# Performance work log

Hardware: AMD Instinct MI355X
Metric: run time of the kernel (lower is better)

The kernel has to match this reference:

```python
import jax, jax.numpy as jnp
import numpy as np

NH0 = 8          # per-head channels (min(max(512//64,2),8))
NHEADS = 4       # assumed einpool head count == number of equivariant eqs
NSTACKS = 4      # max(min(8//2,4),1)
MARGIN = 8.0
F = NH0 * NHEADS  # 32


def _mlp2(x, w1, b1, w2, b2):
    # 2-layer MLP: Linear -> ReLU -> Linear (matches MLP with nlayers=2)
    return jnp.maximum(x @ w1 + b1, 0.0) @ w2 + b2


def _mixed_pool(h, mask):
    # h: (B,C,A,W,F), mask: (B,C,A,W,1)
    B, C, A, W, Fc = h.shape
    # sin-transformed multi-head equivariant einsum pool over axes (a,b)
    y = jnp.sin(h).reshape(B, C, A, W, NH0, NHEADS) * mask[..., None]
    e0 = y[..., 0]                                                        # identity head
    e1 = jnp.broadcast_to(jnp.sum(y[..., 1], axis=3, keepdims=True), e0.shape)  # sum over b
    e2 = jnp.broadcast_to(jnp.sum(y[..., 2], axis=2, keepdims=True), e0.shape)  # sum over a
    e3 = jnp.broadcast_to(jnp.sum(y[..., 3], axis=(2, 3), keepdims=True), e0.shape)  # sum over a,b
    h0 = jnp.concatenate([e0, e1, e2, e3], axis=-1)                       # (B,C,A,W,NH0*4)
    # cascaded 4-way max pool over b, a, C (equivalent to joint max), broadcast back
    h1 = jnp.broadcast_to(jnp.max(h, axis=(1, 2, 3), keepdims=True), h.shape)
    return jnp.concatenate([h0, h1], axis=-1)                             # (B,C,A,W,2F)


def setup_inputs() -> dict:
    key = jax.random.key(0)
    ks = jax.random.split(key, 16)
    B, C, A, W = 8, 24, 96, 96
    nh = 128
    x = jax.random.normal(ks[0], (B, C, A, W), jnp.float32)
    rows_len = jax.random.randint(ks[1], (B, C), 48, A + 1, jnp.int32)
    cols_len = jax.random.randint(ks[2], (B, C), 48, W + 1, jnp.int32)

    def lin(k, fi, fo):
        return jax.random.normal(k, (fi, fo), jnp.float32) / np.float32(np.sqrt(fi))

    inp = {
        'x': x, 'rows_len': rows_len, 'cols_len': cols_len,
        't0_w1': lin(ks[3], 1, nh), 't0_b1': jnp.zeros((nh,), jnp.float32),
        't0_w2': lin(ks[4], nh, F), 't0_b2': jnp.zeros((F,), jnp.float32),
        't_w1': jax.random.normal(ks[5], (NSTACKS, 2 * F, nh), jnp.float32) / np.float32(np.sqrt(2 * F)),
        't_b1': jnp.zeros((NSTACKS, nh), jnp.float32),
        't_w2': jax.random.normal(ks[6], (NSTACKS, nh, F), jnp.float32) / np.float32(np.sqrt(nh)),
        't_b2': jnp.zeros((NSTACKS, F), jnp.float32),
        'tout_w1': lin(ks[7], F, nh), 'tout_b1': jnp.zeros((nh,), jnp.float32),
        'tout_w2': lin(ks[8], nh, 2), 'tout_b2': jnp.zeros((2,), jnp.float32),
    }
    return inp


def reference(x, rows_len, cols_len, t0_w1, t0_b1, t0_w2, t0_b2,
              t_w1, t_b1, t_w2, t_b2, tout_w1, tout_b1, tout_w2, tout_b2):
    B, C, A, W = x.shape
    # ragged validity mask from per-matrix (rows, cols) lengths (nested-tensor pad)
    ra = jnp.arange(A, dtype=jnp.int32)
    rb = jnp.arange(W, dtype=jnp.int32)
    m = ((ra[:, None] < rows_len[..., None, None]) &
         (rb[None, :] < cols_len[..., None, None])).astype(x.dtype)      # (B,C,A,W)
    # per-matrix normalization over valid region (torch .std is unbiased)
    n = jnp.sum(m, axis=(-1, -2), keepdims=True)
    mean = jnp.sum(x * m, axis=(-1, -2), keepdims=True) / jnp.maximum(n, 1.0)
    var = jnp.sum(((x - mean) ** 2) * m, axis=(-1, -2), keepdims=True) / jnp.maximum(n - 1.0, 1.0)
    std = jnp.maximum(jnp.sqrt(var), 1e-12)
    h = (((x - mean) / std) * m)[..., None]                               # (B,C,A,W,1)
    mask = m[..., None]                                                   # (B,C,A,W,1)

    h = _mlp2(h, t0_w1, t0_b1, t0_w2, t0_b2)                              # (B,C,A,W,F)
    for i in range(NSTACKS):
        h = h * mask
        skip = h
        hp = _mixed_pool(h, mask)
        h = skip + _mlp2(hp, t_w1[i], t_b1[i], t_w2[i], t_b2[i])
        h = h * mask

    num = jnp.clip(jnp.sum(h * h, axis=(2, 3)), 1e-20, None)              # (B,C,F)
    den = jnp.clip(jnp.sum(mask, axis=(2, 3)), 1e-12, None)               # (B,C,1)
    h = jnp.sqrt(num / den)
    h = jnp.mean(h, axis=1)                                               # (B,F)
    out = MARGIN * jnp.tanh(_mlp2(h, tout_w1, tout_b1, tout_w2, tout_b2))  # (B,2)
    return out
```

## Files before the change

kernel.cpp:

```cpp
#include <hip/hip_runtime.h>
#include <math.h>
#include <float.h>

#define NB 8
#define NC 24
#define NA 96
#define NW 96
#define NF 32
#define NHID 128
#define AW (NA*NW)
#define NBC (NB*NC)
#define NEL ((size_t)NBC*AW)
#define HSTR 17

typedef float v2f __attribute__((ext_vector_type(2)));
typedef float f32x4 __attribute__((ext_vector_type(4)));
typedef short short8_t __attribute__((ext_vector_type(8)));
#ifndef __has_builtin
#define __has_builtin(x) 0
#endif
#if __has_builtin(__builtin_elementwise_fma)
#define PKFMA(a,b,c) __builtin_elementwise_fma((a),(b),(c))
#else
#define PKFMA(a,b,c) ((a)*(b)+(c))
#endif

union frag_u { unsigned int u[4]; short8_t s; };

__device__ __forceinline__ unsigned short bf16rne(float x) {
    unsigned int u = __float_as_uint(x);
    unsigned int r = u + 0x7fffu + ((u >> 16) & 1u);
    return (unsigned short)(r >> 16);
}
__device__ __forceinline__ float bf2f(unsigned short v) {
    return __uint_as_float(((unsigned int)v) << 16);
}
__device__ __forceinline__ unsigned fkey(float x) {
    unsigned u = __float_as_uint(x);
    return (u >> 31) ? ~u : (u | 0x80000000u);
}
__device__ __forceinline__ float funkey(unsigned k) {
    return (k >> 31) ? __uint_as_float(k ^ 0x80000000u) : __uint_as_float(~k);
}
__device__ __forceinline__ float grp16_sum(float v) {
    v += __shfl_xor(v, 1, 64);
    v += __shfl_xor(v, 2, 64);
    v += __shfl_xor(v, 4, 64);
    v += __shfl_xor(v, 8, 64);
    return v;
}
__device__ __forceinline__ float grp16_max(float v) {
    v = fmaxf(v, __shfl_xor(v, 1, 64));
    v = fmaxf(v, __shfl_xor(v, 2, 64));
    v = fmaxf(v, __shfl_xor(v, 4, 64));
    v = fmaxf(v, __shfl_xor(v, 8, 64));
    return v;
}

__global__ __launch_bounds__(256) void stats_kernel(
    const float* __restrict__ x, const int* __restrict__ rows_len,
    const int* __restrict__ cols_len, float* __restrict__ stats)
{
    int bc = blockIdx.x;
    int R = rows_len[bc], L = cols_len[bc];
    const float* xp = x + (size_t)bc * AW;
    int n = R * L;
    float sx = 0.f, sxx = 0.f;
    for (int i = threadIdx.x; i < n; i += 256) {
        int a = i / L, w = i - a * L;
        float v = xp[a * NW + w];
        sx += v;
        sxx = fmaf(v, v, sxx);
    }
    __shared__ float r1[256], r2[256];
    r1[threadIdx.x] = sx; r2[threadIdx.x] = sxx;
    __syncthreads();
    for (int s = 128; s > 0; s >>= 1) {
        if (threadIdx.x < s) {
            r1[threadIdx.x] += r1[threadIdx.x + s];
            r2[threadIdx.x] += r2[threadIdx.x + s];
        }
        __syncthreads();
    }
    if (threadIdx.x == 0) {
        float fn = (float)n;
        float mean = r1[0] / fn;
        float var = fmaxf((r2[0] - r1[0] * r1[0] / fn) / (fn - 1.f), 0.f);
        float sd = fmaxf(sqrtf(var), 1e-12f);
        stats[2 * bc] = mean;
        stats[2 * bc + 1] = 1.f / sd;
    }
}

__global__ __launch_bounds__(256) void prep_kernel(
    const float* __restrict__ tw1, float* __restrict__ w1t)
{
    int i = blockIdx.x * 256 + threadIdx.x;
    if (i >= 4 * NHID * 24) return;
    int s = i / (NHID * 24), r = i % (NHID * 24);
    int j = r / 24, t = r % 24;
    w1t[i] = tw1[(size_t)s * 64 * NHID + t * NHID + j];
}

__global__ __launch_bounds__(256) void prep2_kernel(
    const float* __restrict__ tw2, unsigned short* __restrict__ w2bf)
{
    int i = blockIdx.x * 256 + threadIdx.x;
    if (i >= 4 * NF * NHID) return;
    int s = i / (NF * NHID), r = i % (NF * NHID);
    int f = r / NHID, j = r % NHID;
    float v = tw2[((size_t)s * NHID + j) * NF + f];
    unsigned short hi = bf16rne(v);
    float hf = bf2f(hi);
    unsigned short lo = bf16rne(v - hf);
    size_t base = (size_t)s * (2 * NF * NHID) + (size_t)f * NHID + j;
    w2bf[base] = hi;
    w2bf[base + NF * NHID] = lo;
}

__global__ __launch_bounds__(256, 4) void t0_kernel(
    const float* __restrict__ x, const int* __restrict__ rows_len,
    const int* __restrict__ cols_len, const float* __restrict__ stats,
    const float* __restrict__ w1, const float* __restrict__ b1,
    const float* __restrict__ w2, const float* __restrict__ b2,
    unsigned short* __restrict__ h, float* __restrict__ rowsum,
    float* __restrict__ colsum, float* __restrict__ matsum,
    unsigned* __restrict__ cmax_key)
{
    __shared__ float col_lds[96 * 9];
    __shared__ float row_lds[8 * 8];
    __shared__ float mat_lds[8];
    __shared__ unsigned max_lds[NF];

    int tid = threadIdx.x;
    int bc = blockIdx.x / 18;
    int base = (blockIdx.x % 18) * 512;
    int lane = tid & 63, wv = tid >> 6;
    int c16 = lane & 15;
    int R = rows_len[bc], L = cols_len[bc];
    float mean = stats[2 * bc], rstd = stats[2 * bc + 1];

    for (int i = tid; i < 96 * 9; i += 256) col_lds[i] = 0.f;
    if (tid < 64) row_lds[tid] = 0.f;
    if (tid < 8) mat_lds[tid] = 0.f;
    if (tid < NF) max_lds[tid] = 0u;

    int eA = base + wv * 128 + lane;
    int eB = eA + 64;
    int aA = eA / NW, wA = eA % NW;
    int aB = eB / NW, wB = eB % NW;
    bool vA = (aA < R) && (wA < L);
    bool vB = (aB < R) && (wB < L);
    size_t gA = (size_t)bc * AW + eA;
    float xA = vA ? (x[gA] - mean) * rstd : 0.f;
    float xB = vB ? (x[gA + 64] - mean) * rstd : 0.f;

    v2f oA[16], oB[16];
    const v2f* b22 = (const v2f*)b2;
    #pragma unroll
    for (int i = 0; i < 16; i++) { v2f bb = b22[i]; oA[i] = bb; oB[i] = bb; }
    for (int j = 0; j < NHID; j++) {
        float hA = fmaxf(fmaf(xA, w1[j], b1[j]), 0.f);
        float hB = fmaxf(fmaf(xB, w1[j], b1[j]), 0.f);
        const v2f* wr = (const v2f*)&w2[j * NF];
        v2f hA2 = {hA, hA}, hB2 = {hB, hB};
        #pragma unroll
        for (int i = 0; i < 16; i++) {
            v2f q = wr[i];
            oA[i] = PKFMA(hA2, q, oA[i]);
            oB[i] = PKFMA(hB2, q, oB[i]);
        }
    }
    float mA = vA ? 1.f : 0.f, mB = vB ? 1.f : 0.f;
    unsigned short* hp = h + (size_t)bc * NF * AW;
    #pragma unroll
    for (int f = 0; f < NF; f++) {
        hp[(size_t)f * AW + eA] = bf16rne(oA[f >> 1][f & 1] * mA);
        hp[(size_t)f * AW + eB] = bf16rne(oB[f >> 1][f & 1] * mB);
    }
    __syncthreads();

    int a0 = base / NW;
    int rowA = aA - a0, rowB = aB - a0;
    float matp[8];
    #pragma unroll
    for (int k = 0; k < 8; k++) matp[k] = 0.f;

    #pragma unroll
    for (int k = 0; k < 8; k++) {
        int fr = 4 * k + 1;
        float sA = grp16_sum(__sinf(oA[fr >> 1][fr & 1] * mA));
        float sB = grp16_sum(__sinf(oB[fr >> 1][fr & 1] * mB));
        if (c16 == 0) {
            atomicAdd(&row_lds[rowA * 8 + k], sA);
            atomicAdd(&row_lds[rowB * 8 + k], sB);
        }
        int fc = 4 * k + 2;
        atomicAdd(&col_lds[wA * 9 + k], __sinf(oA[fc >> 1][fc & 1] * mA));
        atomicAdd(&col_lds[wB * 9 + k], __sinf(oB[fc >> 1][fc & 1] * mB));
        int fm = 4 * k + 3;
        matp[k] = __sinf(oA[fm >> 1][fm & 1] * mA) + __sinf(oB[fm >> 1][fm & 1] * mB);
    }
    #pragma unroll
    for (int k = 0; k < 8; k++) {
        float v = grp16_sum(matp[k]);
        if (c16 == 0) atomicAdd(&mat_lds[k], v);
    }
    #pragma unroll
    for (int f = 0; f < NF; f++) {
        float v = grp16_max(fmaxf(oA[f >> 1][f & 1] * mA, oB[f >> 1][f & 1] * mB));
        if (c16 == 0) atomicMax(&max_lds[f], fkey(v));
    }
    __syncthreads();

    if (tid < 48) {
        int ar = a0 + (tid >> 3);
        if (ar < NA) atomicAdd(&rowsum[(bc * NA + ar) * 8 + (tid & 7)], row_lds[tid]);
    }
    if (tid < 8) atomicAdd(&matsum[bc * 8 + tid], mat_lds[tid]);
    if (tid >= 32 && tid < 64) atomicMax(&cmax_key[bc * NF + tid - 32], max_lds[tid - 32]);
    for (int i = tid; i < NW * 8; i += 256)
        atomicAdd(&colsum[bc * NW * 8 + i], col_lds[(i >> 3) * 9 + (i & 7)]);
}

__global__ __launch_bounds__(256) void precomp_kernel(
    const float* __restrict__ rowsum, const float* __restrict__ colsum,
    const float* __restrict__ matsum, const unsigned* __restrict__ cmax_key,
    const float* __restrict__ w1, const float* __restrict__ b1,
    float* __restrict__ rowc, float* __restrict__ colc)
{
    __shared__ float sbm[NF];
    __shared__ float sconst[NHID];
    __shared__ float scs[NW * 8];
    int tid = threadIdx.x;
    int bc = blockIdx.x, b = bc / NC;

    for (int i = tid; i < NW * 8; i += 256) scs[i] = colsum[bc * NW * 8 + i];
    if (tid < NF) {
        unsigned km = cmax_key[(b * NC) * NF + tid];
        for (int c = 1; c < NC; c++) {
            unsigned kc = cmax_key[(b * NC + c) * NF + tid];
            km = (kc > km) ? kc : km;
        }
        sbm[tid] = funkey(km);
    }
    __syncthreads();
    if (tid < NHID) {
        float v = b1[tid];
        const float* mp = matsum + bc * 8;
        #pragma unroll
        for (int k = 0; k < 8; k++) v = fmaf(mp[k], w1[(24 + k) * NHID + tid], v);
        #pragma unroll
        for (int f = 0; f < NF; f++) v = fmaf(sbm[f], w1[(32 + f) * NHID + tid], v);
        sconst[tid] = v;
    }
    __syncthreads();
    for (int i = tid; i < NHID * NA; i += 256) {
        int j = i / NA, aa = i - j * NA;
        const float* rp = rowsum + (bc * NA + aa) * 8;
        float v = sconst[j];
        #pragma unroll
        for (int k = 0; k < 8; k++) v = fmaf(rp[k], w1[(8 + k) * NHID + j], v);
        rowc[(size_t)bc * (NHID * NA) + i] = v;
    }
    for (int i = tid; i < NHID * NW; i += 256) {
        int j = i / NW, ww = i - j * NW;
        float v = 0.f;
        #pragma unroll
        for (int k = 0; k < 8; k++) v = fmaf(scs[ww * 8 + k], w1[(16 + k) * NHID + j], v);
        colc[(size_t)bc * (NHID * NW) + i] = v;
    }
}

__global__ __launch_bounds__(256, 4) void mlp_kernel(
    unsigned short* __restrict__ h, const float* __restrict__ rowc,
    const float* __restrict__ colc, const int* __restrict__ rows_len,
    const int* __restrict__ cols_len, const float* __restrict__ w1t,
    const unsigned short* __restrict__ w2bf, const float* __restrict__ b2,
    float* __restrict__ sqsum, float* __restrict__ rowsum,
    float* __restrict__ colsum, float* __restrict__ matsum,
    unsigned* __restrict__ cmax_key, int last, int do_pool)
{
    __shared__ unsigned int hid_hi[256 * HSTR];
    __shared__ unsigned int hid_lo[256 * HSTR];

    int tid = threadIdx.x;
    int bc = blockIdx.x / 36;
    int blk36 = blockIdx.x % 36;
    int base = blk36 * 256;
    int lane = tid & 63, wv = tid >> 6;
    int g = lane >> 4, c16 = lane & 15;

    int e = base + tid;
    int a = e / NW, wc = e - a * NW;
    unsigned short* hp = h + (size_t)bc * NF * AW;

    float p[8];
    #pragma unroll
    for (int k = 0; k < 8; k++) p[k] = __sinf(bf2f(hp[(size_t)(4 * k) * AW + e]));
    v2f p2[4];
    #pragma unroll
    for (int t = 0; t < 4; t++) p2[t] = (v2f){p[2 * t], p[2 * t + 1]};

    const unsigned short* w2hi = w2bf;
    const unsigned short* w2lo = w2bf + NF * NHID;

    f32x4 acc[4][2];
    #pragma unroll
    for (int t = 0; t < 2; t++) {
        f32x4 bb = *(const f32x4*)(b2 + 16 * t + 4 * g);
        #pragma unroll
        for (int ti = 0; ti < 4; ti++) acc[ti][t] = bb;
    }

    const float* rcr = rowc + (size_t)bc * (NHID * NA);
    const float* rcc = colc + (size_t)bc * (NHID * NW);

    for (int w = 0; w < 4; w++) {
        int jw = 32 * w;
        frag_u Ah[2], Al[2];
        #pragma unroll
        for (int t = 0; t < 2; t++) {
            size_t off = (size_t)(c16 + 16 * t) * NHID + jw + 8 * g;
            const unsigned int* ph = (const unsigned int*)(w2hi + off);
            const unsigned int* pl = (const unsigned int*)(w2lo + off);
            #pragma unroll
            for (int d = 0; d < 4; d++) { Ah[t].u[d] = ph[d]; Al[t].u[d] = pl[d]; }
        }

        #pragma unroll 4
        for (int jp = 0; jp < 16; jp++) {
            int jl = 2 * jp;
            const v2f* w1r0 = (const v2f*)(w1t + (size_t)(jw + jl) * 24);
            const v2f* w1r1 = w1r0 + 12;
            v2f u0 = {rcr[(size_t)(jw + jl) * NA + a], rcc[(size_t)(jw + jl) * NW + wc]};
            v2f u1 = {rcr[(size_t)(jw + jl + 1) * NA + a], rcc[(size_t)(jw + jl + 1) * NW + wc]};
            #pragma unroll
            for (int t = 0; t < 4; t++) {
                u0 = PKFMA(p2[t], w1r0[t], u0);
                u1 = PKFMA(p2[t], w1r1[t], u1);
            }
            float v0 = fmaxf(u0.x + u0.y, 0.f);
            float v1 = fmaxf(u1.x + u1.y, 0.f);
            unsigned int hi, lo;
            asm("v_cvt_pk_bf16_f32 %0, %1, %2" : "=v"(hi) : "v"(v0), "v"(v1));
            float h0 = __uint_as_float(hi << 16);
            float h1 = __uint_as_float(hi & 0xffff0000u);
            float l0 = v0 - h0, l1 = v1 - h1;
            asm("v_cvt_pk_bf16_f32 %0, %1, %2" : "=v"(lo) : "v"(l0), "v"(l1));
            hid_hi[tid * HSTR + jp] = hi;
            hid_lo[tid * HSTR + jp] = lo;
        }
        __syncthreads();

        #pragma unroll
        for (int ti = 0; ti < 4; ti++) {
            int el = (wv * 4 + ti) * 16 + c16;
            const unsigned int* bh = &hid_hi[el * HSTR + 4 * g];
            const unsigned int* bl = &hid_lo[el * HSTR + 4 * g];
            frag_u Bh, Bl;
            #pragma unroll
            for (int d = 0; d < 4; d++) { Bh.u[d] = bh[d]; Bl.u[d] = bl[d]; }
            #pragma unroll
            for (int t = 0; t < 2; t++) {
                acc[ti][t] = __builtin_amdgcn_mfma_f32_16x16x32_bf16(Ah[t].s, Bh.s, acc[ti][t], 0, 0, 0);
                acc[ti][t] = __builtin_amdgcn_mfma_f32_16x16x32_bf16(Al[t].s, Bh.s, acc[ti][t], 0, 0, 0);
                acc[ti][t] = __builtin_amdgcn_mfma_f32_16x16x32_bf16(Ah[t].s, Bl.s, acc[ti][t], 0, 0, 0);
            }
        }
        __syncthreads();
    }

    float* col_lds = (float*)hid_hi;
    float* row_lds = col_lds + 96 * 9;
    float* mat_lds = row_lds + 32;
    unsigned* max_lds = (unsigned*)(mat_lds + 8);
    if (do_pool) {
        for (int i = tid; i < 96 * 9 + 32 + 8 + 32; i += 256) col_lds[i] = 0.f;
        __syncthreads();
    }

    int R = rows_len[bc], L = cols_len[bc];
    int a0 = base / NW;
    float psum[2][4] = {{0.f, 0.f, 0.f, 0.f}, {0.f, 0.f, 0.f, 0.f}};
    float matp[2] = {0.f, 0.f};
    float mxp[2][4];
    #pragma unroll
    for (int t = 0; t < 2; t++)
        #pragma unroll
        for (int r = 0; r < 4; r++) mxp[t][r] = -FLT_MAX;

    #pragma unroll
    for (int ti = 0; ti < 4; ti++) {
        int el = (wv * 4 + ti) * 16 + c16;
        int ee = base + el;
        int aa = ee / NW, ww = ee - aa * NW;
        float mk = (aa < R && ww < L) ? 1.f : 0.f;
        float rowv[2];
        #pragma unroll
        for (int t = 0; t < 2; t++) {
            #pragma unroll
            for (int r = 0; r < 4; r++) {
                int f = 4 * g + r + 16 * t;
                unsigned short* ad = hp + (size_t)f * AW + ee;
                float hv = (bf2f(*ad) + acc[ti][t][r]) * mk;
                if (!last) *ad = bf16rne(hv);
                else       psum[t][r] = fmaf(hv, hv, psum[t][r]);
                if (do_pool) {
                    mxp[t][r] = fmaxf(mxp[t][r], hv);
                    if (r == 1)      rowv[t] = __sinf(hv);
                    else if (r == 2) atomicAdd(&col_lds[ww * 9 + g + 4 * t], __sinf(hv));
                    else if (r == 3) matp[t] += __sinf(hv);
                }
            }
        }
        if (do_pool) {
            #pragma unroll
            for (int t = 0; t < 2; t++) {
                float v = grp16_sum(rowv[t]);
                if (c16 == 0) atomicAdd(&row_lds[(aa - a0) * 8 + g + 4 * t], v);
            }
        }
    }

    if (do_pool) {
        #pragma unroll
        for (int t = 0; t < 2; t++) {
            float v = grp16_sum(matp[t]);
            if (c16 == 0) atomicAdd(&mat_lds[g + 4 * t], v);
            #pragma unroll
            for (int r = 0; r < 4; r++) {
                float m = grp16_max(mxp[t][r]);
                if (c16 == 0) atomicMax(&max_lds[4 * g + r + 16 * t], fkey(m));
            }
        }
        __syncthreads();
        if (tid < 32) {
            int ar = a0 + (tid >> 3);
            if (ar < NA) atomicAdd(&rowsum[(bc * NA + ar) * 8 + (tid & 7)], row_lds[tid]);
        }
        if (tid < 8) atomicAdd(&matsum[bc * 8 + tid], mat_lds[tid]);
        if (tid >= 32 && tid < 64) atomicMax(&cmax_key[bc * NF + tid - 32], max_lds[tid - 32]);
        for (int i = tid; i < NW * 8; i += 256)
            atomicAdd(&colsum[bc * NW * 8 + i], col_lds[(i >> 3) * 9 + (i & 7)]);
    }

    if (last) {
        float* sq_lds = (float*)hid_hi;
        if (tid < NF) sq_lds[tid] = 0.f;
        __syncthreads();
        #pragma unroll
        for (int t = 0; t < 2; t++) {
            #pragma unroll
            for (int r = 0; r < 4; r++) {
                float v = grp16_sum(psum[t][r]);
                if (c16 == 0) atomicAdd(&sq_lds[4 * g + r + 16 * t], v);
            }
        }
        __syncthreads();
        if (tid < NF) atomicAdd(&sqsum[bc * NF + tid], sq_lds[tid]);
    }
}

__global__ __launch_bounds__(64) void out_kernel(
    const float* __restrict__ sqsum, const int* __restrict__ rows_len,
    const int* __restrict__ cols_len, const float* __restrict__ w1,
    const float* __restrict__ b1, const float* __restrict__ w2,
    const float* __restrict__ b2, float* __restrict__ out)
{
    int b = threadIdx.x;
    if (b >= NB) return;
    float hm[NF];
    #pragma unroll
    for (int f = 0; f < NF; f++) hm[f] = 0.f;
    for (int c = 0; c < NC; c++) {
        int bc = b * NC + c;
        float n = (float)(rows_len[bc] * cols_len[bc]);
        float rdn = 1.f / fmaxf(n, 1e-12f);
        #pragma unroll
        for (int f = 0; f < NF; f++) {
            float q = fmaxf(sqsum[bc * NF + f], 1e-20f);
            hm[f] += sqrtf(q * rdn);
        }
    }
    #pragma unroll
    for (int f = 0; f < NF; f++) hm[f] *= (1.f / (float)NC);

    float o0 = b2[0], o1 = b2[1];
    for (int j = 0; j < NHID; j++) {
        float v = b1[j];
        #pragma unroll
        for (int f = 0; f < NF; f++) v = fmaf(hm[f], w1[f * NHID + j], v);
        v = fmaxf(v, 0.f);
        o0 = fmaf(v, w2[j * 2 + 0], o0);
        o1 = fmaf(v, w2[j * 2 + 1], o1);
    }
    out[b * 2 + 0] = 8.f * tanhf(o0);
    out[b * 2 + 1] = 8.f * tanhf(o1);
}

extern "C" void kernel_launch(void* const* d_in, const int* in_sizes, int n_in,
                              void* d_out, int out_size, void* d_ws, size_t ws_size,
                              hipStream_t stream)
{
    const float* x    = (const float*)d_in[0];
    const int* rl     = (const int*)d_in[1];
    const int* cl     = (const int*)d_in[2];
    const float* t0w1 = (const float*)d_in[3];
    const float* t0b1 = (const float*)d_in[4];
    const float* t0w2 = (const float*)d_in[5];
    const float* t0b2 = (const float*)d_in[6];
    const float* tw1  = (const float*)d_in[7];
    const float* tb1  = (const float*)d_in[8];
    const float* tw2  = (const float*)d_in[9];
    const float* tb2  = (const float*)d_in[10];
    const float* ow1  = (const float*)d_in[11];
    const float* ob1  = (const float*)d_in[12];
    const float* ow2  = (const float*)d_in[13];
    const float* ob2  = (const float*)d_in[14];
    float* out = (float*)d_out;

    float* ws    = (float*)d_ws;
    unsigned short* h = (unsigned short*)ws;
    float* stats = ws + NEL * NF;
    float*    rowb = stats + 2 * NBC;
    float*    matb = rowb + (size_t)NBC * NA * 8;
    unsigned* cmxb = (unsigned*)(matb + NBC * 8);
    float*    colb = (float*)(cmxb + NBC * NF);
    size_t    accum_floats = (size_t)NBC * NA * 8 + NBC * 8 + NBC * NF
                           + (size_t)NBC * NW * 8;
    float* sqb   = colb + (size_t)NBC * NW * 8;
    float* w1tb  = sqb + NBC * NF;
    float* rowcb = w1tb + 4 * NHID * 24;
    float* colcb = rowcb + (size_t)NBC * NHID * NA;
    unsigned short* w2bfb = (unsigned short*)(colcb + (size_t)NBC * NHID * NW);

    hipMemsetAsync(sqb, 0, NBC * NF * sizeof(float), stream);
    hipMemsetAsync(rowb, 0, accum_floats * sizeof(float), stream);
    stats_kernel<<<NBC, 256, 0, stream>>>(x, rl, cl, stats);
    prep_kernel<<<(4 * NHID * 24 + 255) / 256, 256, 0, stream>>>(tw1, w1tb);
    prep2_kernel<<<(4 * NF * NHID + 255) / 256, 256, 0, stream>>>(tw2, w2bfb);
    t0_kernel<<<(int)(NEL / 512), 256, 0, stream>>>(x, rl, cl, stats,
                                                    t0w1, t0b1, t0w2, t0b2, h,
                                                    rowb, colb, matb, cmxb);
    for (int s = 0; s < 4; s++) {
        precomp_kernel<<<NBC, 256, 0, stream>>>(rowb, colb, matb, cmxb,
            tw1 + (size_t)s * 64 * NHID, tb1 + s * NHID, rowcb, colcb);
        if (s < 3)
            hipMemsetAsync(rowb, 0, accum_floats * sizeof(float), stream);
        mlp_kernel<<<NBC * 36, 256, 0, stream>>>(h, rowcb, colcb, rl, cl,
            w1tb + (size_t)s * NHID * 24,
            w2bfb + (size_t)s * (2 * NF * NHID),
            tb2 + s * NF, sqb, rowb, colb, matb, cmxb,
            (s == 3) ? 1 : 0, (s < 3) ? 1 : 0);
    }
    out_kernel<<<1, 64, 0, stream>>>(sqb, rl, cl, ow1, ob1, ow2, ob2, out);
}
```

Baseline: 1.337 ms.

## Move t0 MLP second layer onto bf16 MFMA and specialize last stack kernel

The first-layer MLP kernel used to run its 128x32 second matmul as packed FP32 FMAs in registers, two elements per thread. It now stages the hidden activations in LDS as split hi/lo bf16 pairs and multiplies them with 3-term bf16 MFMA against pre-split t0_w2 weights, one element per thread with twice as many blocks. The stack MLP kernel is also split into separate mid and last variants, so the runtime do_pool and last branches go away and the last stack no longer writes h. The split-bf16 scheme keeps accuracy close to FP32, at the cost of extra LDS traffic and syncs in t0.

Result: faster. 1.201 ms, median of 2 (-10.2%).

```diff
diff --git a/kernel.cpp b/kernel.cpp
--- a/kernel.cpp
+++ b/kernel.cpp
@@ -56,6 +56,14 @@
     v = fmaxf(v, __shfl_xor(v, 8, 64));
     return v;
 }
+__device__ __forceinline__ void pack_hilo(float v0, float v1,
+                                          unsigned int& hi, unsigned int& lo) {
+    asm("v_cvt_pk_bf16_f32 %0, %1, %2" : "=v"(hi) : "v"(v0), "v"(v1));
+    float h0 = __uint_as_float(hi << 16);
+    float h1 = __uint_as_float(hi & 0xffff0000u);
+    float l0 = v0 - h0, l1 = v1 - h1;
+    asm("v_cvt_pk_bf16_f32 %0, %1, %2" : "=v"(lo) : "v"(l0), "v"(l1));
+}
 
 __global__ __launch_bounds__(256) void stats_kernel(
     const float* __restrict__ x, const int* __restrict__ rows_len,
@@ -111,109 +119,159 @@
     int f = r / NHID, j = r % NHID;
     float v = tw2[((size_t)s * NHID + j) * NF + f];
     unsigned short hi = bf16rne(v);
-    float hf = bf2f(hi);
-    unsigned short lo = bf16rne(v - hf);
+    unsigned short lo = bf16rne(v - bf2f(hi));
     size_t base = (size_t)s * (2 * NF * NHID) + (size_t)f * NHID + j;
     w2bf[base] = hi;
     w2bf[base + NF * NHID] = lo;
+}
+
+__global__ __launch_bounds__(256) void prep2t_kernel(
+    const float* __restrict__ t0w2, unsigned short* __restrict__ w2bf)
+{
+    int i = blockIdx.x * 256 + threadIdx.x;
+    if (i >= NF * NHID) return;
+    int f = i / NHID, j = i % NHID;
+    float v = t0w2[(size_t)j * NF + f];
+    unsigned short hi = bf16rne(v);
+    unsigned short lo = bf16rne(v - bf2f(hi));
+    w2bf[(size_t)f * NHID + j] = hi;
+    w2bf[(size_t)NF * NHID + f * NHID + j] = lo;
 }
 
 __global__ __launch_bounds__(256, 4) void t0_kernel(
     const float* __restrict__ x, const int* __restrict__ rows_len,
     const int* __restrict__ cols_len, const float* __restrict__ stats,
     const float* __restrict__ w1, const float* __restrict__ b1,
-    const float* __restrict__ w2, const float* __restrict__ b2,
+    const unsigned short* __restrict__ w2bf, const float* __restrict__ b2,
     unsigned short* __restrict__ h, float* __restrict__ rowsum,
     float* __restrict__ colsum, float* __restrict__ matsum,
     unsigned* __restrict__ cmax_key)
 {
-    __shared__ float col_lds[96 * 9];
-    __shared__ float row_lds[8 * 8];
-    __shared__ float mat_lds[8];
-    __shared__ unsigned max_lds[NF];
+    __shared__ unsigned int hid_hi[256 * HSTR];
+    __shared__ unsigned int hid_lo[256 * HSTR];
 
     int tid = threadIdx.x;
-    int bc = blockIdx.x / 18;
-    int base = (blockIdx.x % 18) * 512;
+    int bc = blockIdx.x / 36;
+    int blk36 = blockIdx.x % 36;
+    int base = blk36 * 256;
     int lane = tid & 63, wv = tid >> 6;
-    int c16 = lane & 15;
+    int g = lane >> 4, c16 = lane & 15;
+
+    int e = base + tid;
+    int a = e / NW, wc = e - a * NW;
     int R = rows_len[bc], L = cols_len[bc];
     float mean = stats[2 * bc], rstd = stats[2 * bc + 1];
-
-    for (int i = tid; i < 96 * 9; i += 256) col_lds[i] = 0.f;
-    if (tid < 64) row_lds[tid] = 0.f;
-    if (tid < 8) mat_lds[tid] = 0.f;
-    if (tid < NF) max_lds[tid] = 0u;
-
-    int eA = base + wv * 128 + lane;
-    int eB = eA + 64;
-    int aA = eA / NW, wA = eA % NW;
-    int aB = eB / NW, wB = eB % NW;
-    bool vA = (aA < R) && (wA < L);
-    bool vB = (aB < R) && (wB < L);
-    size_t gA = (size_t)bc * AW + eA;
-    float xA = vA ? (x[gA] - mean) * rstd : 0.f;
-    float xB = vB ? (x[gA + 64] - mean) * rstd : 0.f;
-
-    v2f oA[16], oB[16];
-    const v2f* b22 = (const v2f*)b2;
-    #pragma unroll
-    for (int i = 0; i < 16; i++) { v2f bb = b22[i]; oA[i] = bb; oB[i] = bb; }
-    for (int j = 0; j < NHID; j++) {
-        float hA = fmaxf(fmaf(xA, w1[j], b1[j]), 0.f);
-        float hB = fmaxf(fmaf(xB, w1[j], b1[j]), 0.f);
-        const v2f* wr = (const v2f*)&w2[j * NF];
-        v2f hA2 = {hA, hA}, hB2 = {hB, hB};
-        #pragma unroll
-        for (int i = 0; i < 16; i++) {
-            v2f q = wr[i];
-            oA[i] = PKFMA(hA2, q, oA[i]);
-            oB[i] = PKFMA(hB2, q, oB[i]);
-        }
-    }
-    float mA = vA ? 1.f : 0.f, mB = vB ? 1.f : 0.f;
+    bool valid = (a < R) && (wc < L);
+    float xn = valid ? (x[(size_t)bc * AW + e] - mean) * rstd : 0.f;
     unsigned short* hp = h + (size_t)bc * NF * AW;
-    #pragma unroll
-    for (int f = 0; f < NF; f++) {
-        hp[(size_t)f * AW + eA] = bf16rne(oA[f >> 1][f & 1] * mA);
-        hp[(size_t)f * AW + eB] = bf16rne(oB[f >> 1][f & 1] * mB);
-    }
+
+    const unsigned short* w2hi = w2bf;
+    const unsigned short* w2lo = w2bf + NF * NHID;
+
+    f32x4 acc[4][2];
+    #pragma unroll
+    for (int t = 0; t < 2; t++) {
+        f32x4 bb = *(const f32x4*)(b2 + 16 * t + 4 * g);
+        #pragma unroll
+        for (int ti = 0; ti < 4; ti++) acc[ti][t] = bb;
+    }
+
+    for (int w = 0; w < 4; w++) {
+        int jw = 32 * w;
+        frag_u Ah[2], Al[2];
+        #pragma unroll
+        for (int t = 0; t < 2; t++) {
+            size_t off = (size_t)(c16 + 16 * t) * NHID + jw + 8 * g;
+            const unsigned int* ph = (const unsigned int*)(w2hi + off);
+            const unsigned int* pl = (const unsigned int*)(w2lo + off);
+            #pragma unroll
+            for (int d = 0; d < 4; d++) { Ah[t].u[d] = ph[d]; Al[t].u[d] = pl[d]; }
+        }
+
+        #pragma unroll 4
+        for (int jp = 0; jp < 16; jp++) {
+            int j0 = jw + 2 * jp;
+            float v0 = fmaxf(fmaf(xn, w1[j0], b1[j0]), 0.f);
+            float v1 = fmaxf(fmaf(xn, w1[j0 + 1], b1[j0 + 1]), 0.f);
+            unsigned int hi, lo;
+            pack_hilo(v0, v1, hi, lo);
+            hid_hi[tid * HSTR + jp] = hi;
+            hid_lo[tid * HSTR + jp] = lo;
+        }
+        __syncthreads();
+
+        #pragma unroll
+        for (int ti = 0; ti < 4; ti++) {
+            int el = (wv * 4 + ti) * 16 + c16;
+            const unsigned int* bh = &hid_hi[el * HSTR + 4 * g];
+            const unsigned int* bl = &hid_lo[el * HSTR + 4 * g];
+            frag_u Bh, Bl;
+            #pragma unroll
+            for (int d = 0; d < 4; d++) { Bh.u[d] = bh[d]; Bl.u[d] = bl[d]; }
+            #pragma unroll
+            for (int t = 0; t < 2; t++) {
+                acc[ti][t] = __builtin_amdgcn_mfma_f32_16x16x32_bf16(Ah[t].s, Bh.s, acc[ti][t], 0, 0, 0);
+                acc[ti][t] = __builtin_amdgcn_mfma_f32_16x16x32_bf16(Al[t].s, Bh.s, acc[ti][t], 0, 0, 0);
+                acc[ti][t] = __builtin_amdgcn_mfma_f32_16x16x32_bf16(Ah[t].s, Bl.s, acc[ti][t], 0, 0, 0);
+            }
+        }
+        __syncthreads();
+    }
+
+    float* col_lds = (float*)hid_hi;
+    float* row_lds = col_lds + 96 * 9;
+    float* mat_lds = row_lds + 32;
+    unsigned* max_lds = (unsigned*)(mat_lds + 8);
+    for (int i = tid; i < 96 * 9 + 32 + 8 + 32; i += 256) col_lds[i] = 0.f;
     __syncthreads();
 
     int a0 = base / NW;
-    int rowA = aA - a0, rowB = aB - a0;
-    float matp[8];
-    #pragma unroll
-    for (int k = 0; k < 8; k++) matp[k] = 0.f;
-
-    #pragma unroll
-    for (int k = 0; k < 8; k++) {
-        int fr = 4 * k + 1;
-        float sA = grp16_sum(__sinf(oA[fr >> 1][fr & 1] * mA));
-        float sB = grp16_sum(__sinf(oB[fr >> 1][fr & 1] * mB));
-        if (c16 == 0) {
-            atomicAdd(&row_lds[rowA * 8 + k], sA);
-            atomicAdd(&row_lds[rowB * 8 + k], sB);
-        }
-        int fc = 4 * k + 2;
-        atomicAdd(&col_lds[wA * 9 + k], __sinf(oA[fc >> 1][fc & 1] * mA));
-        atomicAdd(&col_lds[wB * 9 + k], __sinf(oB[fc >> 1][fc & 1] * mB));
-        int fm = 4 * k + 3;
-        matp[k] = __sinf(oA[fm >> 1][fm & 1] * mA) + __sinf(oB[fm >> 1][fm & 1] * mB);
-    }
-    #pragma unroll
-    for (int k = 0; k < 8; k++) {
-        float v = grp16_sum(matp[k]);
-        if (c16 == 0) atomicAdd(&mat_lds[k], v);
-    }
-    #pragma unroll
-    for (int f = 0; f < NF; f++) {
-        float v = grp16_max(fmaxf(oA[f >> 1][f & 1] * mA, oB[f >> 1][f & 1] * mB));
-        if (c16 == 0) atomicMax(&max_lds[f], fkey(v));
-    }
-    __syncthreads();
-
-    if (tid < 48) {
+    float matp[2] = {0.f, 0.f};
+    float mxp[2][4];
+    #pragma unroll
+    for (int t = 0; t < 2; t++)
+        #pragma unroll
+        for (int r = 0; r < 4; r++) mxp[t][r] = -FLT_MAX;
+
+    #pragma unroll
+    for (int ti = 0; ti < 4; ti++) {
+        int el = (wv * 4 + ti) * 16 + c16;
+        int ee = base + el;
+        int aa = ee / NW, ww = ee - aa * NW;
+        float mk = (aa < R && ww < L) ? 1.f : 0.f;
+        float rowv[2];
+        #pragma unroll
+        for (int t = 0; t < 2; t++) {
+            #pragma unroll
+            for (int r = 0; r < 4; r++) {
+                int f = 4 * g + r + 16 * t;
+                float hv = acc[ti][t][r] * mk;
+                hp[(size_t)f * AW + ee] = bf16rne(hv);
+                mxp[t][r] = fmaxf(mxp[t][r], hv);
+                if (r == 1)      rowv[t] = __sinf(hv);
+                else if (r == 2) atomicAdd(&col_lds[ww * 9 + g + 4 * t], __sinf(hv));
+                else if (r == 3) matp[t] += __sinf(hv);
+            }
+        }
+        #pragma unroll
+        for (int t = 0; t < 2; t++) {
+            float v = grp16_sum(rowv[t]);
+            if (c16 == 0) atomicAdd(&row_lds[(aa - a0) * 8 + g + 4 * t], v);
+        }
+    }
+
+    #pragma unroll
+    for (int t = 0; t < 2; t++) {
+        float v = grp16_sum(matp[t]);
+        if (c16 == 0) atomicAdd(&mat_lds[g + 4 * t], v);
+        #pragma unroll
+        for (int r = 0; r < 4; r++) {
+            float m = grp16_max(mxp[t][r]);
+            if (c16 == 0) atomicMax(&max_lds[4 * g + r + 16 * t], fkey(m));
+        }
+    }
+    __syncthreads();
+    if (tid < 32) {
         int ar = a0 + (tid >> 3);
         if (ar < NA) atomicAdd(&rowsum[(bc * NA + ar) * 8 + (tid & 7)], row_lds[tid]);
     }
@@ -272,29 +330,14 @@
     }
 }
 
-__global__ __launch_bounds__(256, 4) void mlp_kernel(
-    unsigned short* __restrict__ h, const float* __restrict__ rowc,
-    const float* __restrict__ colc, const int* __restrict__ rows_len,
-    const int* __restrict__ cols_len, const float* __restrict__ w1t,
-    const unsigned short* __restrict__ w2bf, const float* __restrict__ b2,
-    float* __restrict__ sqsum, float* __restrict__ rowsum,
-    float* __restrict__ colsum, float* __restrict__ matsum,
-    unsigned* __restrict__ cmax_key, int last, int do_pool)
-{
-    __shared__ unsigned int hid_hi[256 * HSTR];
-    __shared__ unsigned int hid_lo[256 * HSTR];
-
-    int tid = threadIdx.x;
-    int bc = blockIdx.x / 36;
-    int blk36 = blockIdx.x % 36;
-    int base = blk36 * 256;
-    int lane = tid & 63, wv = tid >> 6;
-    int g = lane >> 4, c16 = lane & 15;
-
+__device__ __forceinline__ void mlp_core(
+    int tid, int bc, int base, int a, int wc, int g, int c16, int wv,
+    const unsigned short* hp, const float* rcr, const float* rcc,
+    const float* __restrict__ w1t, const unsigned short* __restrict__ w2bf,
+    const float* __restrict__ b2, unsigned int* hid_hi, unsigned int* hid_lo,
+    f32x4 (&acc)[4][2])
+{
     int e = base + tid;
-    int a = e / NW, wc = e - a * NW;
-    unsigned short* hp = h + (size_t)bc * NF * AW;
-
     float p[8];
     #pragma unroll
     for (int k = 0; k < 8; k++) p[k] = __sinf(bf2f(hp[(size_t)(4 * k) * AW + e]));
@@ -305,16 +348,12 @@
     const unsigned short* w2hi = w2bf;
     const unsigned short* w2lo = w2bf + NF * NHID;
 
-    f32x4 acc[4][2];
     #pragma unroll
     for (int t = 0; t < 2; t++) {
         f32x4 bb = *(const f32x4*)(b2 + 16 * t + 4 * g);
         #pragma unroll
         for (int ti = 0; ti < 4; ti++) acc[ti][t] = bb;
     }
-
-    const float* rcr = rowc + (size_t)bc * (NHID * NA);
-    const float* rcc = colc + (size_t)bc * (NHID * NW);
 
     for (int w = 0; w < 4; w++) {
         int jw = 32 * w;
@@ -343,11 +382,7 @@
             float v0 = fmaxf(u0.x + u0.y, 0.f);
             float v1 = fmaxf(u1.x + u1.y, 0.f);
             unsigned int hi, lo;
-            asm("v_cvt_pk_bf16_f32 %0, %1, %2" : "=v"(hi) : "v"(v0), "v"(v1));
-            float h0 = __uint_as_float(hi << 16);
-            float h1 = __uint_as_float(hi & 0xffff0000u);
-            float l0 = v0 - h0, l1 = v1 - h1;
-            asm("v_cvt_pk_bf16_f32 %0, %1, %2" : "=v"(lo) : "v"(l0), "v"(l1));
+            pack_hilo(v0, v1, hi, lo);
             hid_hi[tid * HSTR + jp] = hi;
             hid_lo[tid * HSTR + jp] = lo;
         }
@@ -370,19 +405,44 @@
         }
         __syncthreads();
     }
+}
+
+__global__ __launch_bounds__(256, 4) void mlp_mid_kernel(
+    unsigned short* __restrict__ h, const float* __restrict__ rowc,
+    const float* __restrict__ colc, const int* __restrict__ rows_len,
+    const int* __restrict__ cols_len, const float* __restrict__ w1t,
+    const unsigned short* __restrict__ w2bf, const float* __restrict__ b2,
+    float* __restrict__ rowsum, float* __restrict__ colsum,
+    float* __restrict__ matsum, unsigned* __restrict__ cmax_key)
+{
+    __shared__ unsigned int hid_hi[256 * HSTR];
+    __shared__ unsigned int hid_lo[256 * HSTR];
+
+    int tid = threadIdx.x;
+    int bc = blockIdx.x / 36;
+    int blk36 = blockIdx.x % 36;
+    int base = blk36 * 256;
+    int lane = tid & 63, wv = tid >> 6;
+    int g = lane >> 4, c16 = lane & 15;
+    int e = base + tid;
+    int a = e / NW, wc = e - a * NW;
+    unsigned short* hp = h + (size_t)bc * NF * AW;
+    const float* rcr = rowc + (size_t)bc * (NHID * NA);
+    const float* rcc = colc + (size_t)bc * (NHID * NW);
+
+    f32x4 acc[4][2];
+    mlp_core(tid, bc, base, a, wc, g, c16, wv, hp, rcr, rcc, w1t, w2bf, b2,
+             hid_hi, hid_lo, acc);
 
     float* col_lds = (float*)hid_hi;
     float* row_lds = col_lds + 96 * 9;
     float* mat_lds = row_lds + 32;
     unsigned* max_lds = (unsigned*)(mat_lds + 8);
-    if (do_pool) {
-        for (int i = tid; i < 96 * 9 + 32 + 8 + 32; i += 256) col_lds[i] = 0.f;
-        __syncthreads();
-    }
+    for (int i = tid; i < 96 * 9 + 32 + 8 + 32; i += 256) col_lds[i] = 0.f;
+    __syncthreads();
 
     int R = rows_len[bc], L = cols_len[bc];
     int a0 = base / NW;
-    float psum[2][4] = {{0.f, 0.f, 0.f, 0.f}, {0.f, 0.f, 0.f, 0.f}};
     float matp[2] = {0.f, 0.f};
     float mxp[2][4];
     #pragma unroll
@@ -404,62 +464,98 @@
                 int f = 4 * g + r + 16 * t;
                 unsigned short* ad = hp + (size_t)f * AW + ee;
                 float hv = (bf2f(*ad) + acc[ti][t][r]) * mk;
-                if (!last) *ad = bf16rne(hv);
-                else       psum[t][r] = fmaf(hv, hv, psum[t][r]);
-                if (do_pool) {
-                    mxp[t][r] = fmaxf(mxp[t][r], hv);
-                    if (r == 1)      rowv[t] = __sinf(hv);
-                    else if (r == 2) atomicAdd(&col_lds[ww * 9 + g + 4 * t], __sinf(hv));
-                    else if (r == 3) matp[t] += __sinf(hv);
-                }
+                *ad = bf16rne(hv);
+                mxp[t][r] = fmaxf(mxp[t][r], hv);
+                if (r == 1)      rowv[t] = __sinf(hv);
+                else if (r == 2) atomicAdd(&col_lds[ww * 9 + g + 4 * t], __sinf(hv));
+                else if (r == 3) matp[t] += __sinf(hv);
             }
         }
-        if (do_pool) {
-            #pragma unroll
-            for (int t = 0; t < 2; t++) {
-                float v = grp16_sum(rowv[t]);
-                if (c16 == 0) atomicAdd(&row_lds[(aa - a0) * 8 + g + 4 * t], v);
+        #pragma unroll
+        for (int t = 0; t < 2; t++) {
+            float v = grp16_sum(rowv[t]);
+            if (c16 == 0) atomicAdd(&row_lds[(aa - a0) * 8 + g + 4 * t], v);
+        }
+    }
+
+    #pragma unroll
+    for (int t = 0; t < 2; t++) {
+        float v = grp16_sum(matp[t]);
+        if (c16 == 0) atomicAdd(&mat_lds[g + 4 * t], v);
+        #pragma unroll
+        for (int r = 0; r < 4; r++) {
+            float m = grp16_max(mxp[t][r]);
+            if (c16 == 0) atomicMax(&max_lds[4 * g + r + 16 * t], fkey(m));
+        }
+    }
+    __syncthreads();
+    if (tid < 32) {
+        int ar = a0 + (tid >> 3);
+        if (ar < NA) atomicAdd(&rowsum[(bc * NA + ar) * 8 + (tid & 7)], row_lds[tid]);
+    }
+    if (tid < 8) atomicAdd(&matsum[bc * 8 + tid], mat_lds[tid]);
+    if (tid >= 32 && tid < 64) atomicMax(&cmax_key[bc * NF + tid - 32], max_lds[tid - 32]);
+    for (int i = tid; i < NW * 8; i += 256)
+        atomicAdd(&colsum[bc * NW * 8 + i], col_lds[(i >> 3) * 9 + (i & 7)]);
+}
+
+__global__ __launch_bounds__(256, 4) void mlp_last_kernel(
+    unsigned short* __restrict__ h, const float* __restrict__ rowc,
+    const float* __restrict__ colc, const int* __restrict__ rows_len,
+    const int* __restrict__ cols_len, const float* __restrict__ w1t,
+    const unsigned short* __restrict__ w2bf, const float* __restrict__ b2,
+    float* __restrict__ sqsum)
+{
+    __shared__ unsigned int hid_hi[256 * HSTR];
+    __shared__ unsigned int hid_lo[256 * HSTR];
+
+    int tid = threadIdx.x;
+    int bc = blockIdx.x / 36;
+    int blk36 = blockIdx.x % 36;
+    int base = blk36 * 256;
+    int lane = tid & 63, wv = tid >> 6;
+    int g = lane >> 4, c16 = lane & 15;
+    int e = base + tid;
+    int a = e / NW, wc = e - a * NW;
+    unsigned short* hp = h + (size_t)bc * NF * AW;
+    const float* rcr = rowc + (size_t)bc * (NHID * NA);
+    const float* rcc = colc + (size_t)bc * (NHID * NW);
+
+    f32x4 acc[4][2];
+    mlp_core(tid, bc, base, a, wc, g, c16, wv, hp, rcr, rcc, w1t, w2bf, b2,
+             hid_hi, hid_lo, acc);
+
+    int R = rows_len[bc], L = cols_len[bc];
+    float psum[2][4] = {{0.f, 0.f, 0.f, 0.f}, {0.f, 0.f, 0.f, 0.f}};
+    #pragma unroll
+    for (int ti = 0; ti < 4; ti++) {
+        int el = (wv * 4 + ti) * 16 + c16;
+        int ee = base + el;
+        int aa = ee / NW, ww = ee - aa * NW;
+        float mk = (aa < R && ww < L) ? 1.f : 0.f;
+        #pragma unroll
+        for (int t = 0; t < 2; t++) {
+            #pragma unroll
+            for (int r = 0; r < 4; r++) {
+                int f = 4 * g + r + 16 * t;
+                float hv = (bf2f(hp[(size_t)f * AW + ee]) + acc[ti][t][r]) * mk;
+                psum[t][r] = fmaf(hv, hv, psum[t][r]);
             }
         }
     }
-
-    if (do_pool) {
-        #pragma unroll
-        for (int t = 0; t < 2; t++) {
-            float v = grp16_sum(matp[t]);
-            if (c16 == 0) atomicAdd(&mat_lds[g + 4 * t], v);
-            #pragma unroll
-            for (int r = 0; r < 4; r++) {
-                float m = grp16_max(mxp[t][r]);
-                if (c16 == 0) atomicMax(&max_lds[4 * g + r + 16 * t], fkey(m));
-            }
-        }
-        __syncthreads();
-        if (tid < 32) {
-            int ar = a0 + (tid >> 3);
-            if (ar < NA) atomicAdd(&rowsum[(bc * NA + ar) * 8 + (tid & 7)], row_lds[tid]);
-        }
-        if (tid < 8) atomicAdd(&matsum[bc * 8 + tid], mat_lds[tid]);
-        if (tid >= 32 && tid < 64) atomicMax(&cmax_key[bc * NF + tid - 32], max_lds[tid - 32]);
-        for (int i = tid; i < NW * 8; i += 256)
-            atomicAdd(&colsum[bc * NW * 8 + i], col_lds[(i >> 3) * 9 + (i & 7)]);
-    }
-
-    if (last) {
-        float* sq_lds = (float*)hid_hi;
-        if (tid < NF) sq_lds[tid] = 0.f;
-        __syncthreads();
-        #pragma unroll
-        for (int t = 0; t < 2; t++) {
-            #pragma unroll
-            for (int r = 0; r < 4; r++) {
-                float v = grp16_sum(psum[t][r]);
-                if (c16 == 0) atomicAdd(&sq_lds[4 * g + r + 16 * t], v);
-            }
-        }
-        __syncthreads();
-        if (tid < NF) atomicAdd(&sqsum[bc * NF + tid], sq_lds[tid]);
-    }
+    float* sq_lds = (float*)hid_hi;
+    if (tid < NF) sq_lds[tid] = 0.f;
+    __syncthreads();
+    #pragma unroll
+    for (int t = 0; t < 2; t++) {
+        #pragma unroll
+        for (int r = 0; r < 4; r++) {
+            float v = grp16_sum(psum[t][r]);
+            if (c16 == 0) atomicAdd(&sq_lds[4 * g + r + 16 * t], v);
+        }
+    }
+    __syncthreads();
+    if (tid < NF) atomicAdd(&sqsum[bc * NF + tid], sq_lds[tid]);
 }
 
 __global__ __launch_bounds__(64) void out_kernel(
@@ -534,25 +630,32 @@
     float* rowcb = w1tb + 4 * NHID * 24;
     float* colcb = rowcb + (size_t)NBC * NHID * NA;
     unsigned short* w2bfb = (unsigned short*)(colcb + (size_t)NBC * NHID * NW);
+    unsigned short* w2t0b = w2bfb + (size_t)4 * 2 * NF * NHID;
 
     hipMemsetAsync(sqb, 0, NBC * NF * sizeof(float), stream);
     hipMemsetAsync(rowb, 0, accum_floats * sizeof(float), stream);
     stats_kernel<<<NBC, 256, 0, stream>>>(x, rl, cl, stats);
     prep_kernel<<<(4 * NHID * 24 + 255) / 256, 256, 0, stream>>>(tw1, w1tb);
     prep2_kernel<<<(4 * NF * NHID + 255) / 256, 256, 0, stream>>>(tw2, w2bfb);
-    t0_kernel<<<(int)(NEL / 512), 256, 0, stream>>>(x, rl, cl, stats,
-                                                    t0w1, t0b1, t0w2, t0b2, h,
-                                                    rowb, colb, matb, cmxb);
+    prep2t_kernel<<<(NF * NHID + 255) / 256, 256, 0, stream>>>(t0w2, w2t0b);
+    t0_kernel<<<NBC * 36, 256, 0, stream>>>(x, rl, cl, stats,
+                                            t0w1, t0b1, w2t0b, t0b2, h,
+                                            rowb, colb, matb, cmxb);
     for (int s = 0; s < 4; s++) {
         precomp_kernel<<<NBC, 256, 0, stream>>>(rowb, colb, matb, cmxb,
             tw1 + (size_t)s * 64 * NHID, tb1 + s * NHID, rowcb, colcb);
-        if (s < 3)
+        if (s < 3) {
             hipMemsetAsync(rowb, 0, accum_floats * sizeof(float), stream);
-        mlp_kernel<<<NBC * 36, 256, 0, stream>>>(h, rowcb, colcb, rl, cl,
-            w1tb + (size_t)s * NHID * 24,
-            w2bfb + (size_t)s * (2 * NF * NHID),
-            tb2 + s * NF, sqb, rowb, colb, matb, cmxb,
-            (s == 3) ? 1 : 0, (s < 3) ? 1 : 0);
+            mlp_mid_kernel<<<NBC * 36, 256, 0, stream>>>(h, rowcb, colcb, rl, cl,
+                w1tb + (size_t)s * NHID * 24,
+                w2bfb + (size_t)s * (2 * NF * NHID),
+                tb2 + s * NF, rowb, colb, matb, cmxb);
+        } else {
+            mlp_last_kernel<<<NBC * 36, 256, 0, stream>>>(h, rowcb, colcb, rl, cl,
+                w1tb + (size_t)s * NHID * 24,
+                w2bfb + (size_t)s * (2 * NF * NHID),
+                tb2 + s * NF, sqb);
+        }
     }
     out_kernel<<<1, 64, 0, stream>>>(sqb, rl, cl, ow1, ob1, ow2, ob2, out);
 }
```
